# Kernel tuning notes

Hardware: AMD Instinct MI355X
Metric: run time of the kernel (lower is better)

Reference implementation:

```python
import jax, jax.numpy as jnp
import numpy as np

LATENT_DIMENSION = 128
HIDDEN = 1024            # HIDDEN_SIZE + LATENT_DIMENSION
SONG_PIECE_SIZE = 128
SONG_LENGTH = 32768
T_STEPS = SONG_LENGTH // SONG_PIECE_SIZE  # 256
BATCH = 128


def setup_inputs() -> dict:
    key = jax.random.key(0)
    ks = jax.random.split(key, 7)
    s_ih = 1.0 / np.sqrt(HIDDEN)
    return {
        "current_batch_size": BATCH,
        "z": jax.random.normal(ks[0], (BATCH, 1, LATENT_DIMENSION), dtype=jnp.float32),
        "w_ih": jax.random.normal(ks[1], (4 * HIDDEN, LATENT_DIMENSION), dtype=jnp.float32) * s_ih,
        "w_hh": jax.random.normal(ks[2], (4 * HIDDEN, HIDDEN), dtype=jnp.float32) * s_ih,
        "b_ih": jax.random.normal(ks[3], (4 * HIDDEN,), dtype=jnp.float32) * s_ih,
        "b_hh": jax.random.normal(ks[4], (4 * HIDDEN,), dtype=jnp.float32) * s_ih,
        "W_fc": jax.random.normal(ks[5], (SONG_PIECE_SIZE, HIDDEN), dtype=jnp.float32) * s_ih,
        "b_fc": jax.random.normal(ks[6], (SONG_PIECE_SIZE,), dtype=jnp.float32) * s_ih,
    }


def _run(z, w_ih, w_hh, b_ih, b_hh, W_fc, b_fc):
    B = z.shape[0]
    # inputs per step: step 0 is z[:,0,:], remaining steps are zeros
    xs = jnp.concatenate(
        [z[:, 0:1, :].transpose(1, 0, 2),
         jnp.zeros((T_STEPS - 1, B, LATENT_DIMENSION), dtype=z.dtype)], axis=0)  # [T,B,L]
    h0 = jnp.zeros((B, HIDDEN), dtype=z.dtype)
    c0 = jnp.zeros((B, HIDDEN), dtype=z.dtype)

    def cell(carry, x):
        h, c = carry
        gates = x @ w_ih.T + b_ih + h @ w_hh.T + b_hh  # [B, 4H]
        i, f, g, o = jnp.split(gates, 4, axis=-1)       # PyTorch gate order i,f,g,o
        c_new = jax.nn.sigmoid(f) * c + jax.nn.sigmoid(i) * jnp.tanh(g)
        h_new = jax.nn.sigmoid(o) * jnp.tanh(c_new)
        y = h_new @ W_fc.T + b_fc                       # [B, SONG_PIECE_SIZE]
        return (h_new, c_new), y

    _, ys = jax.lax.scan(cell, (h0, c0), xs)            # ys: [T, B, P]
    return ys.transpose(1, 0, 2).reshape(B, SONG_LENGTH)


def reference(current_batch_size, z, w_ih, w_hh, b_ih, b_hh, W_fc, b_fc):
    return _run(z, w_ih, w_hh, b_ih, b_hh, W_fc, b_fc)
```

## Files before the change

kernel.cpp:

```cpp
#include <hip/hip_runtime.h>
#include <stdint.h>

#define BB   128
#define LL   128
#define HH   1024
#define G4   4096
#define TT   256
#define PP   128

#define NSL  64
#define NB   256
#define CARSL 56

typedef _Float16 half8  __attribute__((ext_vector_type(8)));
typedef float   floatx4 __attribute__((ext_vector_type(4)));

__device__ __forceinline__ float sigf(float x) {
  x = fminf(fmaxf(x, -30.f), 30.f);
  return 1.f / (1.f + __expf(-x));
}
__device__ __forceinline__ float tanhf_fast(float x) {
  x = fminf(fmaxf(x, -15.f), 15.f);
  float e = __expf(2.f * x);
  return (e - 1.f) / (e + 1.f);
}
__device__ __forceinline__ unsigned short f2h(float x) {
  _Float16 h = (_Float16)x;
  return __builtin_bit_cast(unsigned short, h);
}
__device__ __forceinline__ void store_h(unsigned short* p, float x) {
  __hip_atomic_store(p, f2h(x), __ATOMIC_RELAXED, __HIP_MEMORY_SCOPE_AGENT);
}

#define ALOAD(dst, base, IMM)                                              \
  asm volatile("global_load_dwordx4 %0, %1, off offset:%2 sc0 sc1"         \
               : "=&v"(dst) : "v"(base), "n"(IMM) : "memory")

#define KSTEP(kc, WN)                                                      \
  {                                                                        \
    asm volatile("s_waitcnt vmcnt(%2)"                                     \
                 : "+v"(ap0[(kc) & 15]), "+v"(ap1[(kc) & 15]) : "n"(WN));  \
    half8 a0 = ap0[(kc) & 15], a1 = ap1[(kc) & 15];                        \
    const int sw = ((kc) * 4 + quad) ^ rsw;                                \
    _Pragma("unroll")                                                      \
    for (int nt = 0; nt < NT; ++nt) {                                      \
      half8 b = (nt < NGATE) ? w8[(nt * 16 + l15) * 128 + sw] : fcb[kc];   \
      acc[0][nt] = __builtin_amdgcn_mfma_f32_16x16x32_f16(a0, b, acc[0][nt], 0, 0, 0); \
      acc[1][nt] = __builtin_amdgcn_mfma_f32_16x16x32_f16(a1, b, acc[1][nt], 0, 0, 0); \
    }                                                                      \
    if ((kc) < 16) {                                                       \
      ALOAD(ap0[(kc) & 15], p0, ((kc) + 16) * 64);                         \
      ALOAD(ap1[(kc) & 15], p1, ((kc) + 16) * 64);                         \
    }                                                                      \
  }

__device__ __forceinline__ void stepbar4(unsigned* ctl, int myline, unsigned s) {
  __syncthreads();
  if (threadIdx.x == 0) {
    asm volatile("s_waitcnt vmcnt(0)" ::: "memory");
    __hip_atomic_fetch_add(ctl + myline * 4096, 1u, __ATOMIC_RELAXED,
                           __HIP_MEMORY_SCOPE_AGENT);
    const unsigned tgt = 64u * s;
    for (;;) {
      unsigned a0 = __hip_atomic_load(ctl,          __ATOMIC_RELAXED, __HIP_MEMORY_SCOPE_AGENT);
      unsigned a1 = __hip_atomic_load(ctl + 4096,   __ATOMIC_RELAXED, __HIP_MEMORY_SCOPE_AGENT);
      unsigned a2 = __hip_atomic_load(ctl + 8192,   __ATOMIC_RELAXED, __HIP_MEMORY_SCOPE_AGENT);
      unsigned a3 = __hip_atomic_load(ctl + 12288,  __ATOMIC_RELAXED, __HIP_MEMORY_SCOPE_AGENT);
      unsigned m01 = a0 < a1 ? a0 : a1;
      unsigned m23 = a2 < a3 ? a2 : a3;
      if ((m01 < m23 ? m01 : m23) >= tgt) break;
      __builtin_amdgcn_s_sleep(1);
    }
  }
  __syncthreads();
}

__global__ void prep_gates0(const float* __restrict__ z, const float* __restrict__ w_ih,
                            const float* __restrict__ b_ih, const float* __restrict__ b_hh,
                            float* __restrict__ g0) {
  int j = blockIdx.x;
  int b = threadIdx.x;
  const float* zr = z + b * LL;
  const float* wr = w_ih + (size_t)j * LL;
  float s = 0.f;
#pragma unroll 4
  for (int k = 0; k < LL; ++k) s += zr[k] * wr[k];
  g0[(size_t)b * G4 + j] = s + b_ih[j] + b_hh[j];
}

__global__ void prep_weights(const float* __restrict__ w_hh,
                             unsigned short* __restrict__ wbuf) {
  int R = blockIdx.x;
  int sl = R >> 6, rr = R & 63, tile = rr >> 4, nl = rr & 15;
  int g = (tile == 0) ? 0 : (tile == 1) ? 2 : (tile == 2) ? 1 : 3;
  const float* src = w_hh + (size_t)(g * HH + sl * 16 + nl) * HH;
  int rsw = nl & 7;
  unsigned short* dst = wbuf + (size_t)R * HH;
  for (int k = threadIdx.x; k < HH; k += blockDim.x) {
    int dk = (((k >> 3) ^ rsw) << 3) | (k & 7);
    _Float16 v = (_Float16)src[k];
    dst[dk] = __builtin_bit_cast(unsigned short, v);
  }
}

template <int NT, int NGATE>
__device__ __forceinline__ void gemmK(const unsigned short* __restrict__ hb,
                                      const half8* __restrict__ w8,
                                      const half8 (&fcb)[32],
                                      int au0, int au1,
                                      int quad, int rsw, int l15,
                                      floatx4 acc[2][NT]) {
  const unsigned short* p0 = hb + au0;
  const unsigned short* p1 = hb + au1;
  half8 ap0[16], ap1[16];
  ALOAD(ap0[0],  p0, 0);    ALOAD(ap1[0],  p1, 0);
  ALOAD(ap0[1],  p0, 64);   ALOAD(ap1[1],  p1, 64);
  ALOAD(ap0[2],  p0, 128);  ALOAD(ap1[2],  p1, 128);
  ALOAD(ap0[3],  p0, 192);  ALOAD(ap1[3],  p1, 192);
  ALOAD(ap0[4],  p0, 256);  ALOAD(ap1[4],  p1, 256);
  ALOAD(ap0[5],  p0, 320);  ALOAD(ap1[5],  p1, 320);
  ALOAD(ap0[6],  p0, 384);  ALOAD(ap1[6],  p1, 384);
  ALOAD(ap0[7],  p0, 448);  ALOAD(ap1[7],  p1, 448);
  ALOAD(ap0[8],  p0, 512);  ALOAD(ap1[8],  p1, 512);
  ALOAD(ap0[9],  p0, 576);  ALOAD(ap1[9],  p1, 576);
  ALOAD(ap0[10], p0, 640);  ALOAD(ap1[10], p1, 640);
  ALOAD(ap0[11], p0, 704);  ALOAD(ap1[11], p1, 704);
  ALOAD(ap0[12], p0, 768);  ALOAD(ap1[12], p1, 768);
  ALOAD(ap0[13], p0, 832);  ALOAD(ap1[13], p1, 832);
  ALOAD(ap0[14], p0, 896);  ALOAD(ap1[14], p1, 896);
  ALOAD(ap0[15], p0, 960);  ALOAD(ap1[15], p1, 960);
  KSTEP(0, 30)  KSTEP(1, 30)  KSTEP(2, 30)  KSTEP(3, 30)
  KSTEP(4, 30)  KSTEP(5, 30)  KSTEP(6, 30)  KSTEP(7, 30)
  KSTEP(8, 30)  KSTEP(9, 30)  KSTEP(10, 30) KSTEP(11, 30)
  KSTEP(12, 30) KSTEP(13, 30) KSTEP(14, 30) KSTEP(15, 30)
  KSTEP(16, 30) KSTEP(17, 28) KSTEP(18, 26) KSTEP(19, 24)
  KSTEP(20, 22) KSTEP(21, 20) KSTEP(22, 18) KSTEP(23, 16)
  KSTEP(24, 14) KSTEP(25, 12) KSTEP(26, 10) KSTEP(27, 8)
  KSTEP(28, 6)  KSTEP(29, 4)  KSTEP(30, 2)  KSTEP(31, 0)
}

__global__ __launch_bounds__(64, 1) void lstm_persist(
    const float* __restrict__ g0,
    const unsigned short* __restrict__ wbuf,
    const float* __restrict__ b_ih, const float* __restrict__ b_hh,
    const float* __restrict__ W_fc, const float* __restrict__ b_fc,
    float* __restrict__ out,
    unsigned short* __restrict__ hbuf,
    unsigned* __restrict__ ctl) {
  extern __shared__ __align__(16) unsigned short sW[];
  const int tid  = threadIdx.x;
  const int lane = tid;
  const int quad = lane >> 4;
  const int l15  = lane & 15;
  const int bid  = blockIdx.x;
  const int sl   = bid >> 2;
  const int q    = bid & 3;
  const int mbase = q * 32;
  const int rsw  = l15 & 7;
  const bool carrier = (sl >= CARSL);
  const int pcol = (sl - CARSL) * 16 + l15;

  {
    const uint4* s4 = (const uint4*)(wbuf + (size_t)sl * 64 * HH);
    uint4* d4 = (uint4*)sW;
    for (int i = tid; i < 64 * HH / 8; i += 64) d4[i] = s4[i];
  }
  __syncthreads();
  const half8* w8 = (const half8*)sW;
  const floatx4 z4 = {0.f, 0.f, 0.f, 0.f};

  half8 fcb[32];
  float biasf = 0.f;
  if (carrier) {
    biasf = b_fc[pcol];
    const float* wp = W_fc + (size_t)pcol * HH + quad * 8;
#pragma unroll
    for (int kc = 0; kc < 32; ++kc) {
      float4 f0 = *(const float4*)(wp + kc * 32);
      float4 f1 = *(const float4*)(wp + kc * 32 + 4);
      half8 hv;
      hv[0] = (_Float16)f0.x; hv[1] = (_Float16)f0.y;
      hv[2] = (_Float16)f0.z; hv[3] = (_Float16)f0.w;
      hv[4] = (_Float16)f1.x; hv[5] = (_Float16)f1.y;
      hv[6] = (_Float16)f1.z; hv[7] = (_Float16)f1.w;
      fcb[kc] = hv;
    }
  }

  const int u = sl * 16 + l15;
  const float bi = b_ih[u]          + b_hh[u];
  const float bf = b_ih[HH + u]     + b_hh[HH + u];
  const float bg = b_ih[2*HH + u]   + b_hh[2*HH + u];
  const float bo = b_ih[3*HH + u]   + b_hh[3*HH + u];
  float c[2][4] = {{0,0,0,0},{0,0,0,0}};

#pragma unroll
  for (int mt = 0; mt < 2; ++mt)
#pragma unroll
    for (int r = 0; r < 4; ++r) {
      const int m = mbase + mt * 16 + quad * 4 + r;
      const float* gr = g0 + (size_t)m * G4;
      float iv = gr[u], gv = gr[2 * HH + u], ov = gr[3 * HH + u];
      float ct = sigf(iv) * tanhf_fast(gv);
      c[mt][r] = ct;
      store_h(hbuf + (size_t)m * HH + u, sigf(ov) * tanhf_fast(ct));
    }
  stepbar4(ctl, bid & 3, 1u);

  const int au0 = (mbase +      l15) * HH + quad * 8;
  const int au1 = (mbase + 16 + l15) * HH + quad * 8;

  if (carrier) {
    for (int t = 1; t < TT; ++t) {
      const unsigned short* hb = hbuf + (size_t)((t - 1) & 1) * BB * HH;
      unsigned short* hw = hbuf + (size_t)(t & 1) * BB * HH;
      floatx4 acc[2][5] = {{z4, z4, z4, z4, z4}, {z4, z4, z4, z4, z4}};
      gemmK<5, 4>(hb, w8, fcb, au0, au1, quad, rsw, l15, acc);
#pragma unroll
      for (int mt = 0; mt < 2; ++mt)
#pragma unroll
        for (int r = 0; r < 4; ++r) {
          float iv = sigf(acc[mt][0][r] + bi);
          float gv = tanhf_fast(acc[mt][1][r] + bg);
          float fv = sigf(acc[mt][2][r] + bf);
          float ov = sigf(acc[mt][3][r] + bo);
          float ct = fv * c[mt][r] + iv * gv;
          c[mt][r] = ct;
          const int m = mbase + mt * 16 + quad * 4 + r;
          store_h(hw + (size_t)m * HH + u, ov * tanhf_fast(ct));
          out[(size_t)m * (TT * PP) + (size_t)(t - 1) * PP + pcol] =
              acc[mt][4][r] + biasf;
        }
      stepbar4(ctl, bid & 3, (unsigned)(t + 1));
    }
    {
      const unsigned short* hb = hbuf + (size_t)((TT - 1) & 1) * BB * HH;
      floatx4 acc[2][1] = {{z4}, {z4}};
      gemmK<1, 0>(hb, w8, fcb, au0, au1, quad, rsw, l15, acc);
#pragma unroll
      for (int mt = 0; mt < 2; ++mt)
#pragma unroll
        for (int r = 0; r < 4; ++r) {
          const int m = mbase + mt * 16 + quad * 4 + r;
          out[(size_t)m * (TT * PP) + (size_t)(TT - 1) * PP + pcol] =
              acc[mt][0][r] + biasf;
        }
    }
  } else {
    for (int t = 1; t < TT; ++t) {
      const unsigned short* hb = hbuf + (size_t)((t - 1) & 1) * BB * HH;
      unsigned short* hw = hbuf + (size_t)(t & 1) * BB * HH;
      floatx4 acc[2][4] = {{z4, z4, z4, z4}, {z4, z4, z4, z4}};
      gemmK<4, 4>(hb, w8, fcb, au0, au1, quad, rsw, l15, acc);
#pragma unroll
      for (int mt = 0; mt < 2; ++mt)
#pragma unroll
        for (int r = 0; r < 4; ++r) {
          float iv = sigf(acc[mt][0][r] + bi);
          float gv = tanhf_fast(acc[mt][1][r] + bg);
          float fv = sigf(acc[mt][2][r] + bf);
          float ov = sigf(acc[mt][3][r] + bo);
          float ct = fv * c[mt][r] + iv * gv;
          c[mt][r] = ct;
          const int m = mbase + mt * 16 + quad * 4 + r;
          store_h(hw + (size_t)m * HH + u, ov * tanhf_fast(ct));
        }
      stepbar4(ctl, bid & 3, (unsigned)(t + 1));
    }
  }
}

extern "C" void kernel_launch(void* const* d_in, const int* in_sizes, int n_in,
                              void* d_out, int out_size, void* d_ws, size_t ws_size,
                              hipStream_t stream) {
  const float* z    = (const float*)d_in[1];
  const float* w_ih = (const float*)d_in[2];
  const float* w_hh = (const float*)d_in[3];
  const float* b_ih = (const float*)d_in[4];
  const float* b_hh = (const float*)d_in[5];
  const float* W_fc = (const float*)d_in[6];
  const float* b_fc = (const float*)d_in[7];
  float* out = (float*)d_out;

  char* ws = (char*)d_ws;
  unsigned*       ctl  = (unsigned*)ws;
  unsigned short* hbuf = (unsigned short*)(ws + 65536);
  float*          g0   = (float*)(ws + 65536 + (size_t)2 * BB * HH * 2);
  unsigned short* wbuf = (unsigned short*)(ws + 65536 + (size_t)2 * BB * HH * 2
                                              + (size_t)BB * G4 * 4);

  (void)hipFuncSetAttribute(reinterpret_cast<const void*>(lstm_persist),
                            hipFuncAttributeMaxDynamicSharedMemorySize, 160 * 1024);

  hipMemsetAsync(ctl, 0, 65536, stream);
  prep_gates0 <<<dim3(G4), dim3(BB), 0, stream>>>(z, w_ih, b_ih, b_hh, g0);
  prep_weights<<<dim3(NSL * 64), dim3(256), 0, stream>>>(w_hh, wbuf);
  lstm_persist<<<dim3(NB), dim3(64), 128 * 1024, stream>>>(g0, wbuf, b_ih, b_hh,
                                                           W_fc, b_fc, out, hbuf, ctl);
}
```

Baseline: 2.503 ms.

## Replace counter barrier with per-slice flag publish and wave-wide poll

Swaps the global atomic-add barrier, which spins on four shared counters, for per-block step flags. Each block stores its step number to its own slot and waits with a 64-lane load plus __all before reading the previous hidden state, so no RMW atomics or __syncthreads are needed. The wait only covers the 64 slices of the same batch quarter, which removes contention and waiting on unrelated quarters. The risk is visibility: the double-buffered h now relies on relaxed store/load ordering and per-quarter dependence only, and the ctl slots must be zeroed and laid out to match.

Result: faster. 2.349 ms (-6.1%).

```diff
diff --git a/kernel.cpp b/kernel.cpp
--- a/kernel.cpp
+++ b/kernel.cpp
@@ -54,25 +54,17 @@
     }                                                                      \
   }
 
-__device__ __forceinline__ void stepbar4(unsigned* ctl, int myline, unsigned s) {
-  __syncthreads();
-  if (threadIdx.x == 0) {
-    asm volatile("s_waitcnt vmcnt(0)" ::: "memory");
-    __hip_atomic_fetch_add(ctl + myline * 4096, 1u, __ATOMIC_RELAXED,
-                           __HIP_MEMORY_SCOPE_AGENT);
-    const unsigned tgt = 64u * s;
-    for (;;) {
-      unsigned a0 = __hip_atomic_load(ctl,          __ATOMIC_RELAXED, __HIP_MEMORY_SCOPE_AGENT);
-      unsigned a1 = __hip_atomic_load(ctl + 4096,   __ATOMIC_RELAXED, __HIP_MEMORY_SCOPE_AGENT);
-      unsigned a2 = __hip_atomic_load(ctl + 8192,   __ATOMIC_RELAXED, __HIP_MEMORY_SCOPE_AGENT);
-      unsigned a3 = __hip_atomic_load(ctl + 12288,  __ATOMIC_RELAXED, __HIP_MEMORY_SCOPE_AGENT);
-      unsigned m01 = a0 < a1 ? a0 : a1;
-      unsigned m23 = a2 < a3 ? a2 : a3;
-      if ((m01 < m23 ? m01 : m23) >= tgt) break;
-      __builtin_amdgcn_s_sleep(1);
-    }
-  }
-  __syncthreads();
+__device__ __forceinline__ void publish(unsigned* qf, int sl, unsigned v, int lane) {
+  asm volatile("s_waitcnt vmcnt(0)" ::: "memory");
+  if (lane == 0)
+    __hip_atomic_store(qf + sl, v, __ATOMIC_RELAXED, __HIP_MEMORY_SCOPE_AGENT);
+}
+__device__ __forceinline__ void waitq(const unsigned* qf, unsigned tgt, int lane) {
+  for (;;) {
+    unsigned v = __hip_atomic_load(qf + lane, __ATOMIC_RELAXED, __HIP_MEMORY_SCOPE_AGENT);
+    if (__all(v >= tgt)) break;
+    __builtin_amdgcn_s_sleep(1);
+  }
 }
 
 __global__ void prep_gates0(const float* __restrict__ z, const float* __restrict__ w_ih,
@@ -160,6 +152,8 @@
   const bool carrier = (sl >= CARSL);
   const int pcol = (sl - CARSL) * 16 + l15;
 
+  unsigned* qf = ctl + q * 1024;
+
   {
     const uint4* s4 = (const uint4*)(wbuf + (size_t)sl * 64 * HH);
     uint4* d4 = (uint4*)sW;
@@ -205,13 +199,14 @@
       c[mt][r] = ct;
       store_h(hbuf + (size_t)m * HH + u, sigf(ov) * tanhf_fast(ct));
     }
-  stepbar4(ctl, bid & 3, 1u);
+  publish(qf, sl, 1u, lane);
 
   const int au0 = (mbase +      l15) * HH + quad * 8;
   const int au1 = (mbase + 16 + l15) * HH + quad * 8;
 
   if (carrier) {
     for (int t = 1; t < TT; ++t) {
+      waitq(qf, (unsigned)t, lane);
       const unsigned short* hb = hbuf + (size_t)((t - 1) & 1) * BB * HH;
       unsigned short* hw = hbuf + (size_t)(t & 1) * BB * HH;
       floatx4 acc[2][5] = {{z4, z4, z4, z4, z4}, {z4, z4, z4, z4, z4}};
@@ -231,8 +226,9 @@
           out[(size_t)m * (TT * PP) + (size_t)(t - 1) * PP + pcol] =
               acc[mt][4][r] + biasf;
         }
-      stepbar4(ctl, bid & 3, (unsigned)(t + 1));
-    }
+      publish(qf, sl, (unsigned)(t + 1), lane);
+    }
+    waitq(qf, (unsigned)TT, lane);
     {
       const unsigned short* hb = hbuf + (size_t)((TT - 1) & 1) * BB * HH;
       floatx4 acc[2][1] = {{z4}, {z4}};
@@ -248,6 +244,7 @@
     }
   } else {
     for (int t = 1; t < TT; ++t) {
+      waitq(qf, (unsigned)t, lane);
       const unsigned short* hb = hbuf + (size_t)((t - 1) & 1) * BB * HH;
       unsigned short* hw = hbuf + (size_t)(t & 1) * BB * HH;
       floatx4 acc[2][4] = {{z4, z4, z4, z4}, {z4, z4, z4, z4}};
@@ -265,7 +262,7 @@
           const int m = mbase + mt * 16 + quad * 4 + r;
           store_h(hw + (size_t)m * HH + u, ov * tanhf_fast(ct));
         }
-      stepbar4(ctl, bid & 3, (unsigned)(t + 1));
+      publish(qf, sl, (unsigned)(t + 1), lane);
     }
   }
 }
```
